# Performance work log

Measured on AMD Instinct MI355X. Metric: run time of the kernel, lower is better.

## Reference

```python
import jax, jax.numpy as jnp
import numpy as np
import math

B, S, DIM = 2, 2048, 2048
N_HEADS, N_KV_HEADS = 32, 8
HEAD_DIM = DIM // N_HEADS  # 64
N_REP = N_HEADS // N_KV_HEADS  # 4
NEG_INF = -1e9


def setup_inputs() -> dict:
    key = jax.random.key(0)
    ks = jax.random.split(key, 6)
    x = jax.random.normal(ks[0], (B, S, DIM), dtype=jnp.float32)
    # RoPE frequencies (standard Llama formulation)
    inv_freq = 1.0 / (10000.0 ** (np.arange(0, HEAD_DIM, 2, dtype=np.float32) / HEAD_DIM))
    t = np.arange(S, dtype=np.float32)
    freqs = np.outer(t, inv_freq)  # [S, HEAD_DIM//2]
    freqs_cos = jnp.asarray(np.cos(freqs), dtype=jnp.float32)
    freqs_sin = jnp.asarray(np.sin(freqs), dtype=jnp.float32)
    # additive causal mask [S, S]
    mask = jnp.where(jnp.tril(jnp.ones((S, S), dtype=bool)), 0.0, NEG_INF).astype(jnp.float32)
    sc = 1.0 / math.sqrt(DIM)
    wq = jax.random.normal(ks[1], (DIM, N_HEADS * HEAD_DIM), dtype=jnp.float32) * sc
    wk = jax.random.normal(ks[2], (DIM, N_KV_HEADS * HEAD_DIM), dtype=jnp.float32) * sc
    wv = jax.random.normal(ks[3], (DIM, N_KV_HEADS * HEAD_DIM), dtype=jnp.float32) * sc
    wo = jax.random.normal(ks[4], (N_HEADS * HEAD_DIM, DIM), dtype=jnp.float32) * sc
    return {"x": x, "freqs_cos": freqs_cos, "freqs_sin": freqs_sin, "mask": mask,
            "wq": wq, "wk": wk, "wv": wv, "wo": wo}


def _apply_rotary(x, cos, sin):
    # x: [B, S, H, HEAD_DIM]; cos/sin: [S, HEAD_DIM//2]
    b, s, h, d = x.shape
    xr = x.astype(jnp.float32).reshape(b, s, h, d // 2, 2)
    xe, xo = xr[..., 0], xr[..., 1]
    c = cos[None, :, None, :]
    sn = sin[None, :, None, :]
    oe = xe * c - xo * sn
    oo = xe * sn + xo * c
    out = jnp.stack([oe, oo], axis=-1).reshape(b, s, h, d)
    return out.astype(x.dtype)


def reference(x, freqs_cos, freqs_sin, mask, wq, wk, wv, wo):
    b, s, _ = x.shape
    xq = (x @ wq).reshape(b, s, N_HEADS, HEAD_DIM)
    xk = (x @ wk).reshape(b, s, N_KV_HEADS, HEAD_DIM)
    xv = (x @ wv).reshape(b, s, N_KV_HEADS, HEAD_DIM)
    xq = _apply_rotary(xq, freqs_cos, freqs_sin)
    xk = _apply_rotary(xk, freqs_cos, freqs_sin)
    # repeat_kv: [B, S, KVH, D] -> [B, S, H, D]
    keys = jnp.repeat(xk, N_REP, axis=2)
    values = jnp.repeat(xv, N_REP, axis=2)
    # [B, H, Q, K] scores (naive, materialized as in source)
    scores = jnp.einsum('bqhd,bkhd->bhqk', xq, keys) / math.sqrt(HEAD_DIM)
    scores = scores + mask[None, None, :, :]
    probs = jax.nn.softmax(scores.astype(jnp.float32), axis=-1).astype(xq.dtype)
    out = jnp.einsum('bhqk,bkhd->bqhd', probs, values).reshape(b, s, N_HEADS * HEAD_DIM)
    return out @ wo
```

## Files before the change

kernel.cpp:

```cpp
#include <hip/hip_runtime.h>
#include <hip/hip_bf16.h>

typedef __bf16 bf16x8 __attribute__((ext_vector_type(8)));
typedef float f32x4 __attribute__((ext_vector_type(4)));
typedef float f32x16 __attribute__((ext_vector_type(16)));
typedef short s16x4 __attribute__((ext_vector_type(4)));
typedef short s16x8 __attribute__((ext_vector_type(8)));

__device__ __forceinline__ short f2bf(float f) {
  union { __bf16 h; short s; } p; p.h = (__bf16)f; return p.s;
}
__device__ __forceinline__ float bf2f(short s) {
  union { unsigned u; float f; } v; v.u = ((unsigned)(unsigned short)s) << 16;
  return v.f;
}
__device__ __forceinline__ void gload16(const void* g, void* l) {
  __builtin_amdgcn_global_load_lds(
      (const __attribute__((address_space(1))) unsigned*)g,
      (__attribute__((address_space(3))) unsigned*)l, 16, 0, 0);
}
__device__ __forceinline__ unsigned pack2(float lo, float hi) {
  union { __bf16 h[2]; unsigned u; } p;
  p.h[0] = (__bf16)lo; p.h[1] = (__bf16)hi;
  return p.u;
}
__device__ __forceinline__ float vmax16(const f32x16& v) {
  const float a0 = fmaxf(v[0], v[1]), a1 = fmaxf(v[2], v[3]);
  const float a2 = fmaxf(v[4], v[5]), a3 = fmaxf(v[6], v[7]);
  const float a4 = fmaxf(v[8], v[9]), a5 = fmaxf(v[10], v[11]);
  const float a6 = fmaxf(v[12], v[13]), a7 = fmaxf(v[14], v[15]);
  const float b0 = fmaxf(a0, a1), b1 = fmaxf(a2, a3);
  const float b2 = fmaxf(a4, a5), b3 = fmaxf(a6, a7);
  return fmaxf(fmaxf(b0, b1), fmaxf(b2, b3));
}
__device__ __forceinline__ float vsum16(const f32x16& v) {
  const float a0 = v[0] + v[1], a1 = v[2] + v[3], a2 = v[4] + v[5], a3 = v[6] + v[7];
  const float a4 = v[8] + v[9], a5 = v[10] + v[11], a6 = v[12] + v[13], a7 = v[14] + v[15];
  return ((a0 + a1) + (a2 + a3)) + ((a4 + a5) + (a6 + a7));
}

constexpr float KSC = 0.18033688f;

__global__ __launch_bounds__(256) void prep_kernel(const float* __restrict__ x,
                                                   const float* __restrict__ wq,
                                                   const float* __restrict__ wk,
                                                   const float* __restrict__ wv,
                                                   const float* __restrict__ wo,
                                                   short* __restrict__ xb,
                                                   short* __restrict__ wqT,
                                                   short* __restrict__ wkT,
                                                   short* __restrict__ wvT,
                                                   short* __restrict__ woT) {
  __shared__ float T[32][33];
  const int z = blockIdx.z;
  if (z == 4) {
    const int bid = blockIdx.y * 64 + blockIdx.x;
    const int i0 = bid * 512 + threadIdx.x;
    #pragma unroll
    for (int q = 0; q < 2; ++q) {
      const int i = i0 + q * 256;
      const float4 v = reinterpret_cast<const float4*>(x)[i];
      s16x4 o;
      o[0] = f2bf(v.x); o[1] = f2bf(v.y); o[2] = f2bf(v.z); o[3] = f2bf(v.w);
      reinterpret_cast<s16x4*>(xb)[i] = o;
    }
    return;
  }
  const float* W; short* WT; int N;
  if (z == 0)      { W = wq; WT = wqT; N = 2048; }
  else if (z == 1) { W = wk; WT = wkT; N = 512; }
  else if (z == 2) { W = wv; WT = wvT; N = 512; }
  else             { W = wo; WT = woT; N = 2048; }
  const int k0 = blockIdx.x * 32, n0 = blockIdx.y * 32;
  if (n0 >= N) return;
  const int r = threadIdx.x >> 5, c = threadIdx.x & 31;
  #pragma unroll
  for (int q = 0; q < 4; ++q) T[r + q * 8][c] = W[(size_t)(k0 + r + q * 8) * N + n0 + c];
  __syncthreads();
  #pragma unroll
  for (int q = 0; q < 4; ++q)
    WT[(size_t)(n0 + r + q * 8) * 2048 + k0 + c] = f2bf(T[c][r + q * 8]);
}

__device__ __forceinline__ void rope_apply(short* __restrict__ X, const float* __restrict__ cosT,
                                           const float* __restrict__ sinT, int i, int shift,
                                           float scale) {
  const int s = (i >> shift) & 2047;
  const int p0 = (i & 7) * 4;
  s16x8 v = *reinterpret_cast<const s16x8*>(&X[(size_t)i * 8]);
  #pragma unroll
  for (int jj = 0; jj < 4; ++jj) {
    const float c = cosT[s * 32 + p0 + jj];
    const float sn = sinT[s * 32 + p0 + jj];
    const float e = bf2f(v[2 * jj]), o = bf2f(v[2 * jj + 1]);
    v[2 * jj] = f2bf((e * c - o * sn) * scale);
    v[2 * jj + 1] = f2bf((e * sn + o * c) * scale);
  }
  *reinterpret_cast<s16x8*>(&X[(size_t)i * 8]) = v;
}

__global__ void rope_both(short* __restrict__ Q, short* __restrict__ K,
                          const float* __restrict__ cosT, const float* __restrict__ sinT) {
  const int i = blockIdx.x * blockDim.x + threadIdx.x;
  if (i < 1048576) rope_apply(Q, cosT, sinT, i, 8, KSC);
  else             rope_apply(K, cosT, sinT, i - 1048576, 6, 1.0f);
}

template <int EPI>
__global__ __launch_bounds__(256) void gemm_tn(const short* __restrict__ A,
                                               const short* __restrict__ BT,
                                               void* __restrict__ C0,
                                               void* __restrict__ C1,
                                               void* __restrict__ C2,
                                               int M, int N, int K) {
  __shared__ short As[128 * 64];
  __shared__ short Bs[128 * 64];
  const int tid = threadIdx.x, lane = tid & 63, wid = tid >> 6;
  const int row0 = blockIdx.x * 128, col0 = blockIdx.y * 128;
  const int wr = (wid >> 1) * 64, wc = (wid & 1) * 64;
  const int lr = lane & 15, lk = (lane >> 4) * 8;
  f32x4 acc[4][4] = {};

  for (int k0 = 0; k0 < K; k0 += 64) {
    #pragma unroll
    for (int i = 0; i < 4; ++i) {
      const int c = i * 256 + tid, r = c >> 3, ch = (c & 7) * 8;
      gload16(&A[(size_t)(row0 + r) * K + k0 + ch], &As[r * 64 + ch]);
      gload16(&BT[(size_t)(col0 + r) * K + k0 + ch], &Bs[r * 64 + ch]);
    }
    __syncthreads();
    #pragma unroll
    for (int kk = 0; kk < 64; kk += 32) {
      bf16x8 af[4], bfr[4];
      #pragma unroll
      for (int m = 0; m < 4; ++m)
        af[m] = *reinterpret_cast<const bf16x8*>(&As[(wr + m * 16 + lr) * 64 + kk + lk]);
      #pragma unroll
      for (int n = 0; n < 4; ++n)
        bfr[n] = *reinterpret_cast<const bf16x8*>(&Bs[(wc + n * 16 + lr) * 64 + kk + lk]);
      #pragma unroll
      for (int m = 0; m < 4; ++m)
        #pragma unroll
        for (int n = 0; n < 4; ++n)
          acc[m][n] = __builtin_amdgcn_mfma_f32_16x16x32_bf16(af[m], bfr[n], acc[m][n], 0, 0, 0);
    }
    __syncthreads();
  }

  const int lc = lane & 15, lr4 = (lane >> 4) * 4;
  if constexpr (EPI == 1) {
    #pragma unroll
    for (int m = 0; m < 4; ++m)
      #pragma unroll
      for (int n = 0; n < 4; ++n)
        #pragma unroll
        for (int i = 0; i < 4; ++i) {
          const int row = row0 + wr + m * 16 + lr4 + i;
          const int col = col0 + wc + n * 16 + lc;
          ((float*)C0)[(size_t)row * N + col] = acc[m][n][i];
        }
  } else {
    #pragma unroll
    for (int m = 0; m < 4; ++m) {
      #pragma unroll
      for (int n = 0; n < 4; ++n) {
        const int row = row0 + wr + m * 16 + lr4;
        const int col = col0 + wc + n * 16 + lc;
        if (col0 < 2048) {
          #pragma unroll
          for (int i = 0; i < 4; ++i)
            ((short*)C0)[(size_t)(row + i) * 2048 + col] = f2bf(acc[m][n][i]);
        } else if (col0 < 2560) {
          #pragma unroll
          for (int i = 0; i < 4; ++i)
            ((short*)C1)[(size_t)(row + i) * 512 + (col - 2048)] = f2bf(acc[m][n][i]);
        } else {
          const int c2 = col - 2560;
          const int kvh = c2 >> 6, d = c2 & 63;
          const int bb = row >> 11, st = row & 2047;
          s16x4 o4;
          #pragma unroll
          for (int i = 0; i < 4; ++i) o4[i] = f2bf(acc[m][n][i]);
          *reinterpret_cast<s16x4*>(
              &((short*)C2)[((size_t)(bb * 8 + kvh) * 64 + d) * 2048 + st]) = o4;
        }
      }
    }
  }
}


template <bool MASKED>
__device__ __forceinline__ void ptile(const short* __restrict__ Ksb,
                                      const short* __restrict__ Vsb,
                                      const bf16x8 qf[4], int kb, int qrow,
                                      int l31, int hi,
                                      f32x16& o0, f32x16& o1, float& m_r, float& l_r) {
  f32x16 sa0 = {}, sa1 = {};
  __builtin_amdgcn_s_setprio(1);
  #pragma unroll
  for (int ds = 0; ds < 4; ++ds) {
    const int c0 = ((ds * 2 + hi) ^ (l31 & 7)) * 8;
    const bf16x8 kf0 = *reinterpret_cast<const bf16x8*>(&Ksb[l31 * 64 + c0]);
    const bf16x8 kf1 = *reinterpret_cast<const bf16x8*>(&Ksb[(32 + l31) * 64 + c0]);
    sa0 = __builtin_amdgcn_mfma_f32_32x32x16_bf16(kf0, qf[ds], sa0, 0, 0, 0);
    sa1 = __builtin_amdgcn_mfma_f32_32x32x16_bf16(kf1, qf[ds], sa1, 0, 0, 0);
  }
  __builtin_amdgcn_s_setprio(0);
  if (MASKED) {
    #pragma unroll
    for (int r = 0; r < 16; ++r) {
      const int kk = kb + (r & 3) + 8 * (r >> 2) + 4 * hi;
      if (kk > qrow) sa0[r] = -1e30f;
      if (kk + 32 > qrow) sa1[r] = -1e30f;
    }
  }
  float mx = fmaxf(vmax16(sa0), vmax16(sa1));
  mx = fmaxf(mx, __shfl_xor(mx, 32, 64));
  if (!__all(mx <= m_r + 8.0f)) {
    const float mn = fmaxf(m_r, mx);
    const float sc = exp2f(m_r - mn);
    #pragma unroll
    for (int r = 0; r < 16; ++r) { o0[r] *= sc; o1[r] *= sc; }
    l_r *= sc;
    m_r = mn;
  }
  #pragma unroll
  for (int r = 0; r < 16; ++r) {
    sa0[r] = exp2f(sa0[r] - m_r);
    sa1[r] = exp2f(sa1[r] - m_r);
  }
  l_r += vsum16(sa0) + vsum16(sa1);
  bf16x8 paf[4];
  #pragma unroll
  for (int ks = 0; ks < 4; ++ks) {
    union { unsigned w[4]; bf16x8 v; } u;
    #pragma unroll
    for (int w2 = 0; w2 < 4; ++w2) {
      const int rbase = (ks & 1) * 8 + w2 * 2;
      if (ks < 2) u.w[w2] = pack2(sa0[rbase], sa0[rbase + 1]);
      else        u.w[w2] = pack2(sa1[rbase], sa1[rbase + 1]);
    }
    paf[ks] = u.v;
  }
  __builtin_amdgcn_s_setprio(1);
  #pragma unroll
  for (int ks = 0; ks < 4; ++ks) {
    const int g0 = ((2 * ks) ^ (l31 & 7)) * 8 + hi * 4;
    const int g1 = ((2 * ks + 1) ^ (l31 & 7)) * 8 + hi * 4;
    union { s16x4 h2[2]; bf16x8 v; } a0, a1;
    a0.h2[0] = *reinterpret_cast<const s16x4*>(&Vsb[l31 * 64 + g0]);
    a0.h2[1] = *reinterpret_cast<const s16x4*>(&Vsb[l31 * 64 + g1]);
    a1.h2[0] = *reinterpret_cast<const s16x4*>(&Vsb[(32 + l31) * 64 + g0]);
    a1.h2[1] = *reinterpret_cast<const s16x4*>(&Vsb[(32 + l31) * 64 + g1]);
    o0 = __builtin_amdgcn_mfma_f32_32x32x16_bf16(a0.v, paf[ks], o0, 0, 0, 0);
    o1 = __builtin_amdgcn_mfma_f32_32x32x16_bf16(a1.v, paf[ks], o1, 0, 0, 0);
  }
  __builtin_amdgcn_s_setprio(0);
}

template <bool MA>
__device__ __forceinline__ void ptile2(const short* __restrict__ Ksb,
                                       const short* __restrict__ Vsb,
                                       const bf16x8 qfA[4], const bf16x8 qfB[4],
                                       int kb, int qrowA, int l31, int hi,
                                       f32x16& oA0, f32x16& oA1, f32x16& oB0, f32x16& oB1,
                                       float& mA, float& lA, float& mB, float& lB) {
  f32x16 a0 = {}, a1 = {}, b0 = {}, b1 = {};
  __builtin_amdgcn_s_setprio(1);
  #pragma unroll
  for (int ds = 0; ds < 4; ++ds) {
    const int c0 = ((ds * 2 + hi) ^ (l31 & 7)) * 8;
    const bf16x8 kf0 = *reinterpret_cast<const bf16x8*>(&Ksb[l31 * 64 + c0]);
    const bf16x8 kf1 = *reinterpret_cast<const bf16x8*>(&Ksb[(32 + l31) * 64 + c0]);
    a0 = __builtin_amdgcn_mfma_f32_32x32x16_bf16(kf0, qfA[ds], a0, 0, 0, 0);
    b0 = __builtin_amdgcn_mfma_f32_32x32x16_bf16(kf0, qfB[ds], b0, 0, 0, 0);
    a1 = __builtin_amdgcn_mfma_f32_32x32x16_bf16(kf1, qfA[ds], a1, 0, 0, 0);
    b1 = __builtin_amdgcn_mfma_f32_32x32x16_bf16(kf1, qfB[ds], b1, 0, 0, 0);
  }
  __builtin_amdgcn_s_setprio(0);
  if (MA) {
    #pragma unroll
    for (int r = 0; r < 16; ++r) {
      const int kk = kb + (r & 3) + 8 * (r >> 2) + 4 * hi;
      if (kk > qrowA) a0[r] = -1e30f;
      if (kk + 32 > qrowA) a1[r] = -1e30f;
    }
  }
  float mxA = fmaxf(vmax16(a0), vmax16(a1));
  float mxB = fmaxf(vmax16(b0), vmax16(b1));
  mxA = fmaxf(mxA, __shfl_xor(mxA, 32, 64));
  mxB = fmaxf(mxB, __shfl_xor(mxB, 32, 64));
  if (!__all(mxA <= mA + 8.0f)) {
    const float mn = fmaxf(mA, mxA);
    const float sc = exp2f(mA - mn);
    #pragma unroll
    for (int r = 0; r < 16; ++r) { oA0[r] *= sc; oA1[r] *= sc; }
    lA *= sc; mA = mn;
  }
  if (!__all(mxB <= mB + 8.0f)) {
    const float mn = fmaxf(mB, mxB);
    const float sc = exp2f(mB - mn);
    #pragma unroll
    for (int r = 0; r < 16; ++r) { oB0[r] *= sc; oB1[r] *= sc; }
    lB *= sc; mB = mn;
  }
  #pragma unroll
  for (int r = 0; r < 16; ++r) {
    a0[r] = exp2f(a0[r] - mA);
    b0[r] = exp2f(b0[r] - mB);
    a1[r] = exp2f(a1[r] - mA);
    b1[r] = exp2f(b1[r] - mB);
  }
  lA += vsum16(a0) + vsum16(a1);
  lB += vsum16(b0) + vsum16(b1);
  bf16x8 pafA[4], pafB[4];
  #pragma unroll
  for (int ks = 0; ks < 4; ++ks) {
    union { unsigned w[4]; bf16x8 v; } ua, ub;
    #pragma unroll
    for (int w2 = 0; w2 < 4; ++w2) {
      const int rbase = (ks & 1) * 8 + w2 * 2;
      if (ks < 2) { ua.w[w2] = pack2(a0[rbase], a0[rbase + 1]);
                    ub.w[w2] = pack2(b0[rbase], b0[rbase + 1]); }
      else        { ua.w[w2] = pack2(a1[rbase], a1[rbase + 1]);
                    ub.w[w2] = pack2(b1[rbase], b1[rbase + 1]); }
    }
    pafA[ks] = ua.v; pafB[ks] = ub.v;
  }
  __builtin_amdgcn_s_setprio(1);
  #pragma unroll
  for (int ks = 0; ks < 4; ++ks) {
    const int g0 = ((2 * ks) ^ (l31 & 7)) * 8 + hi * 4;
    const int g1 = ((2 * ks + 1) ^ (l31 & 7)) * 8 + hi * 4;
    union { s16x4 h2[2]; bf16x8 v; } v0, v1;
    v0.h2[0] = *reinterpret_cast<const s16x4*>(&Vsb[l31 * 64 + g0]);
    v0.h2[1] = *reinterpret_cast<const s16x4*>(&Vsb[l31 * 64 + g1]);
    v1.h2[0] = *reinterpret_cast<const s16x4*>(&Vsb[(32 + l31) * 64 + g0]);
    v1.h2[1] = *reinterpret_cast<const s16x4*>(&Vsb[(32 + l31) * 64 + g1]);
    oA0 = __builtin_amdgcn_mfma_f32_32x32x16_bf16(v0.v, pafA[ks], oA0, 0, 0, 0);
    oB0 = __builtin_amdgcn_mfma_f32_32x32x16_bf16(v0.v, pafB[ks], oB0, 0, 0, 0);
    oA1 = __builtin_amdgcn_mfma_f32_32x32x16_bf16(v1.v, pafA[ks], oA1, 0, 0, 0);
    oB1 = __builtin_amdgcn_mfma_f32_32x32x16_bf16(v1.v, pafB[ks], oB1, 0, 0, 0);
  }
  __builtin_amdgcn_s_setprio(0);
}

__global__ __launch_bounds__(512, 2) void attn3(const short* __restrict__ Q,
                                                const short* __restrict__ K,
                                                const short* __restrict__ VT,
                                                short* __restrict__ O) {
  constexpr int S = 2048, H = 32;
  const int pair = blockIdx.x, kvh = blockIdx.y, b = blockIdx.z;
  const int tid = threadIdx.x, lane = tid & 63, wid = tid >> 6;
  const int hg = wid & 3, rowhalf = wid >> 2;
  const int h = kvh * 4 + hg;
  const int l31 = lane & 31, hi = lane >> 5;
  const int qpA = pair, qpB = 31 - pair;
  const int q0A = qpA * 64 + rowhalf * 32, q0B = qpB * 64 + rowhalf * 32;
  const int qrowA = q0A + l31, qrowB = q0B + l31;
  const int bk = b * 8 + kvh;

  __shared__ short Ks[2][8192];
  __shared__ short Vs[2][8192];

  bf16x8 qfA[4], qfB[4];
  {
    const size_t qa = ((size_t)(b * S + qrowA) * H + h) * 64;
    const size_t qb = ((size_t)(b * S + qrowB) * H + h) * 64;
    #pragma unroll
    for (int ds = 0; ds < 4; ++ds) {
      qfA[ds] = *reinterpret_cast<const bf16x8*>(&Q[qa + ds * 16 + hi * 8]);
      qfB[ds] = *reinterpret_cast<const bf16x8*>(&Q[qb + ds * 16 + hi * 8]);
    }
  }

  f32x16 oA0 = {}, oA1 = {}, oB0 = {}, oB1 = {};
  float mA = -1e30f, lA = 0.f, mB = -1e30f, lB = 0.f;

  const int njt = (qpB + 2) >> 1;
  const size_t kroot = ((size_t)b * S * 8 + kvh) * 64;
  const size_t vroot = (size_t)bk * 64 * S;

  const int sr = tid >> 3, sch = tid & 7;
  const int cs8 = (sch ^ (sr & 7)) * 8;

  auto stage = [&](int j, int buf) {
    #pragma unroll
    for (int s = 0; s < 2; ++s) {
      gload16(&K[kroot + (size_t)(j * 128 + s * 64 + sr) * 512 + cs8],
              &Ks[buf][s * 4096 + tid * 8]);
      gload16(&VT[vroot + (size_t)sr * S + j * 128 + s * 64 + cs8],
              &Vs[buf][s * 4096 + tid * 8]);
    }
  };

  stage(0, 0);
  __syncthreads();

  int cur = 0;
  for (int j = 0; j < njt; ++j) {
    if (j + 1 < njt) stage(j + 1, cur ^ 1);
    #pragma unroll
    for (int s = 0; s < 2; ++s) {
      const int kb = j * 128 + s * 64;
      const short* Ksb = &Ks[cur][s * 4096];
      const short* Vsb = &Vs[cur][s * 4096];
      if (kb <= q0A + 31) {
        if (kb + 63 <= q0A)
          ptile2<false>(Ksb, Vsb, qfA, qfB, kb, qrowA, l31, hi,
                        oA0, oA1, oB0, oB1, mA, lA, mB, lB);
        else
          ptile2<true>(Ksb, Vsb, qfA, qfB, kb, qrowA, l31, hi,
                       oA0, oA1, oB0, oB1, mA, lA, mB, lB);
      } else if (kb <= q0B + 31) {
        if (kb + 63 <= q0B)
          ptile<false>(Ksb, Vsb, qfB, kb, qrowB, l31, hi, oB0, oB1, mB, lB);
        else
          ptile<true>(Ksb, Vsb, qfB, kb, qrowB, l31, hi, oB0, oB1, mB, lB);
      }
    }
    __syncthreads();
    cur ^= 1;
  }

  lA += __shfl_xor(lA, 32, 64);
  lB += __shfl_xor(lB, 32, 64);
  {
    const float inv = 1.f / lA;
    const size_t obase = ((size_t)(b * S + qrowA) * H + h) * 64;
    #pragma unroll
    for (int g = 0; g < 4; ++g) {
      s16x4 s0v, s1v;
      #pragma unroll
      for (int i = 0; i < 4; ++i) {
        s0v[i] = f2bf(oA0[4 * g + i] * inv);
        s1v[i] = f2bf(oA1[4 * g + i] * inv);
      }
      *reinterpret_cast<s16x4*>(&O[obase + 8 * g + 4 * hi]) = s0v;
      *reinterpret_cast<s16x4*>(&O[obase + 32 + 8 * g + 4 * hi]) = s1v;
    }
  }
  {
    const float inv = 1.f / lB;
    const size_t obase = ((size_t)(b * S + qrowB) * H + h) * 64;
    #pragma unroll
    for (int g = 0; g < 4; ++g) {
      s16x4 s0v, s1v;
      #pragma unroll
      for (int i = 0; i < 4; ++i) {
        s0v[i] = f2bf(oB0[4 * g + i] * inv);
        s1v[i] = f2bf(oB1[4 * g + i] * inv);
      }
      *reinterpret_cast<s16x4*>(&O[obase + 8 * g + 4 * hi]) = s0v;
      *reinterpret_cast<s16x4*>(&O[obase + 32 + 8 * g + 4 * hi]) = s1v;
    }
  }
}

extern "C" void kernel_launch(void* const* d_in, const int* in_sizes, int n_in,
                              void* d_out, int out_size, void* d_ws, size_t ws_size,
                              hipStream_t stream) {
  const float* x  = (const float*)d_in[0];
  const float* fc = (const float*)d_in[1];
  const float* fs = (const float*)d_in[2];
  const float* wq = (const float*)d_in[4];
  const float* wk = (const float*)d_in[5];
  const float* wv = (const float*)d_in[6];
  const float* wo = (const float*)d_in[7];
  float* out = (float*)d_out;

  short* xb  = (short*)d_ws;
  short* wqT = xb  + 8388608;
  short* wkT = wqT + 4194304;
  short* wvT = wkT + 1048576;
  short* woT = wvT + 1048576;
  short* Qb  = woT + 4194304;
  short* Kb  = Qb  + 8388608;
  short* VTb = Kb  + 2097152;
  short* attb = xb;

  prep_kernel<<<dim3(64, 64, 5), 256, 0, stream>>>(x, wq, wk, wv, wo,
                                                   xb, wqT, wkT, wvT, woT);

  gemm_tn<3><<<dim3(32, 24), 256, 0, stream>>>(xb, wqT, Qb, Kb, VTb, 4096, 3072, 2048);

  rope_both<<<5120, 256, 0, stream>>>(Qb, Kb, fc, fs);

  attn3<<<dim3(16, 8, 2), 512, 0, stream>>>(Qb, Kb, VTb, attb);

  gemm_tn<1><<<dim3(32, 16), 256, 0, stream>>>(attb, woT, out, nullptr, nullptr, 4096, 2048, 2048);
}
```

Baseline: 257.2 us.

## Rewrite projection GEMMs with larger tiles, LDS double buffering, swizzle and block remap

Replaces the 128x128 single-buffered GEMM with a 512-thread kernel using 256-wide N tiles (BM 256 for QKV, 128 for output), double-buffered LDS so the next K-tile loads overlap MFMA work, and XOR-swizzled LDS layout to avoid bank conflicts. It also remaps block IDs across XCD-style groups of 8 and raises MFMA priority. Larger tiles cut global traffic per flop but use much more LDS and registers, and the grids shrink to 192 and 256 blocks, which can underfill the 256 CUs.

```diff
diff --git a/kernel.cpp b/kernel.cpp
--- a/kernel.cpp
+++ b/kernel.cpp
@@ -106,66 +106,103 @@
   else             rope_apply(K, cosT, sinT, i - 1048576, 6, 1.0f);
 }
 
-template <int EPI>
-__global__ __launch_bounds__(256) void gemm_tn(const short* __restrict__ A,
-                                               const short* __restrict__ BT,
-                                               void* __restrict__ C0,
-                                               void* __restrict__ C1,
-                                               void* __restrict__ C2,
-                                               int M, int N, int K) {
-  __shared__ short As[128 * 64];
-  __shared__ short Bs[128 * 64];
+template <int BM, int EPI>
+__global__ __launch_bounds__(512, 2) void gemm256(const short* __restrict__ A,
+                                                  const short* __restrict__ BT,
+                                                  void* __restrict__ C0,
+                                                  void* __restrict__ C1,
+                                                  void* __restrict__ C2,
+                                                  int M, int N, int K) {
+  constexpr int BN = 256, BK = 64;
+  constexpr int AIT = (BM * 8) / 512;
+  constexpr int MREP = BM / 32;
+  __shared__ short As[2][BM * BK];
+  __shared__ short Bs[2][BN * BK];
   const int tid = threadIdx.x, lane = tid & 63, wid = tid >> 6;
-  const int row0 = blockIdx.x * 128, col0 = blockIdx.y * 128;
-  const int wr = (wid >> 1) * 64, wc = (wid & 1) * 64;
-  const int lr = lane & 15, lk = (lane >> 4) * 8;
-  f32x4 acc[4][4] = {};
-
-  for (int k0 = 0; k0 < K; k0 += 64) {
-    #pragma unroll
-    for (int i = 0; i < 4; ++i) {
-      const int c = i * 256 + tid, r = c >> 3, ch = (c & 7) * 8;
-      gload16(&A[(size_t)(row0 + r) * K + k0 + ch], &As[r * 64 + ch]);
-      gload16(&BT[(size_t)(col0 + r) * K + k0 + ch], &Bs[r * 64 + ch]);
-    }
+  const int wm = wid >> 2, wn = wid & 3;
+  const int lr = lane & 15, hi2 = lane >> 4;
+
+  const int nwg = gridDim.x * gridDim.y;
+  int bid = blockIdx.y * gridDim.x + blockIdx.x;
+  bid = (bid & 7) * (nwg >> 3) + (bid >> 3);
+  const int row0 = (bid % gridDim.x) * BM;
+  const int col0 = (bid / gridDim.x) * BN;
+
+  size_t aSrc[AIT]; int aDst[AIT];
+  size_t bSrc[4];   int bDst[4];
+  #pragma unroll
+  for (int i = 0; i < AIT; ++i) {
+    const int c = i * 512 + tid, r = c >> 3, ch = c & 7;
+    aSrc[i] = (size_t)(row0 + r) * K + (ch ^ (r & 7)) * 8;
+    aDst[i] = c * 8;
+  }
+  #pragma unroll
+  for (int i = 0; i < 4; ++i) {
+    const int c = i * 512 + tid, r = c >> 3, ch = c & 7;
+    bSrc[i] = (size_t)(col0 + r) * K + (ch ^ (r & 7)) * 8;
+    bDst[i] = c * 8;
+  }
+
+  f32x4 acc[MREP][4] = {};
+
+  const int NT = K / BK;
+  #pragma unroll
+  for (int i = 0; i < AIT; ++i) gload16(&A[aSrc[i]], &As[0][aDst[i]]);
+  #pragma unroll
+  for (int i = 0; i < 4; ++i) gload16(&BT[bSrc[i]], &Bs[0][bDst[i]]);
+
+  int buf = 0;
+  for (int t = 0; t < NT; ++t) {
     __syncthreads();
-    #pragma unroll
-    for (int kk = 0; kk < 64; kk += 32) {
-      bf16x8 af[4], bfr[4];
-      #pragma unroll
-      for (int m = 0; m < 4; ++m)
-        af[m] = *reinterpret_cast<const bf16x8*>(&As[(wr + m * 16 + lr) * 64 + kk + lk]);
+    if (t + 1 < NT) {
+      const int k1 = (t + 1) * BK;
+      #pragma unroll
+      for (int i = 0; i < AIT; ++i) gload16(&A[aSrc[i] + k1], &As[buf ^ 1][aDst[i]]);
+      #pragma unroll
+      for (int i = 0; i < 4; ++i) gload16(&BT[bSrc[i] + k1], &Bs[buf ^ 1][bDst[i]]);
+    }
+    #pragma unroll
+    for (int ks = 0; ks < 2; ++ks) {
+      const int sw = ((ks * 4 + hi2) ^ (lr & 7)) * 8;
+      bf16x8 af[MREP], bfr[4];
+      #pragma unroll
+      for (int m = 0; m < MREP; ++m)
+        af[m] = *reinterpret_cast<const bf16x8*>(
+            &As[buf][(wm * (BM / 2) + m * 16 + lr) * BK + sw]);
       #pragma unroll
       for (int n = 0; n < 4; ++n)
-        bfr[n] = *reinterpret_cast<const bf16x8*>(&Bs[(wc + n * 16 + lr) * 64 + kk + lk]);
-      #pragma unroll
-      for (int m = 0; m < 4; ++m)
+        bfr[n] = *reinterpret_cast<const bf16x8*>(
+            &Bs[buf][(wn * 64 + n * 16 + lr) * BK + sw]);
+      __builtin_amdgcn_s_setprio(1);
+      #pragma unroll
+      for (int m = 0; m < MREP; ++m)
         #pragma unroll
         for (int n = 0; n < 4; ++n)
           acc[m][n] = __builtin_amdgcn_mfma_f32_16x16x32_bf16(af[m], bfr[n], acc[m][n], 0, 0, 0);
-    }
-    __syncthreads();
+      __builtin_amdgcn_s_setprio(0);
+    }
+    buf ^= 1;
   }
 
   const int lc = lane & 15, lr4 = (lane >> 4) * 4;
   if constexpr (EPI == 1) {
     #pragma unroll
-    for (int m = 0; m < 4; ++m)
+    for (int m = 0; m < MREP; ++m)
       #pragma unroll
       for (int n = 0; n < 4; ++n)
         #pragma unroll
         for (int i = 0; i < 4; ++i) {
-          const int row = row0 + wr + m * 16 + lr4 + i;
-          const int col = col0 + wc + n * 16 + lc;
+          const int row = row0 + wm * (BM / 2) + m * 16 + lr4 + i;
+          const int col = col0 + wn * 64 + n * 16 + lc;
           ((float*)C0)[(size_t)row * N + col] = acc[m][n][i];
         }
   } else {
     #pragma unroll
-    for (int m = 0; m < 4; ++m) {
+    for (int m = 0; m < MREP; ++m) {
       #pragma unroll
       for (int n = 0; n < 4; ++n) {
-        const int row = row0 + wr + m * 16 + lr4;
-        const int col = col0 + wc + n * 16 + lc;
+        const int row = row0 + wm * (BM / 2) + m * 16 + lr4;
+        const int col = col0 + wn * 64 + n * 16 + lc;
         if (col0 < 2048) {
           #pragma unroll
           for (int i = 0; i < 4; ++i)
@@ -189,7 +226,6 @@
   }
 }
 
-
 template <bool MASKED>
 __device__ __forceinline__ void ptile(const short* __restrict__ Ksb,
                                       const short* __restrict__ Vsb,
@@ -385,13 +421,13 @@
   const int sr = tid >> 3, sch = tid & 7;
   const int cs8 = (sch ^ (sr & 7)) * 8;
 
-  auto stage = [&](int j, int buf) {
+  auto stage = [&](int j, int bufi) {
     #pragma unroll
     for (int s = 0; s < 2; ++s) {
       gload16(&K[kroot + (size_t)(j * 128 + s * 64 + sr) * 512 + cs8],
-              &Ks[buf][s * 4096 + tid * 8]);
+              &Ks[bufi][s * 4096 + tid * 8]);
       gload16(&VT[vroot + (size_t)sr * S + j * 128 + s * 64 + cs8],
-              &Vs[buf][s * 4096 + tid * 8]);
+              &Vs[bufi][s * 4096 + tid * 8]);
     }
   };
 
@@ -483,11 +519,11 @@
   prep_kernel<<<dim3(64, 64, 5), 256, 0, stream>>>(x, wq, wk, wv, wo,
                                                    xb, wqT, wkT, wvT, woT);
 
-  gemm_tn<3><<<dim3(32, 24), 256, 0, stream>>>(xb, wqT, Qb, Kb, VTb, 4096, 3072, 2048);
+  gemm256<256, 3><<<dim3(16, 12), 512, 0, stream>>>(xb, wqT, Qb, Kb, VTb, 4096, 3072, 2048);
 
   rope_both<<<5120, 256, 0, stream>>>(Qb, Kb, fc, fs);
 
   attn3<<<dim3(16, 8, 2), 512, 0, stream>>>(Qb, Kb, VTb, attb);
 
-  gemm_tn<1><<<dim3(32, 16), 256, 0, stream>>>(attb, woT, out, nullptr, nullptr, 4096, 2048, 2048);
-}
+  gemm256<128, 1><<<dim3(32, 8), 512, 0, stream>>>(attb, woT, out, nullptr, nullptr, 4096, 2048, 2048);
+}
```

Result: faster. 236.8 us (-8.0%).
